# Kernel tuning notes

Hardware: AMD Instinct MI355X
Metric: run time of the kernel (lower is better)

## Reference

```python
import jax, jax.numpy as jnp
import numpy as np

N, E = 50000, 800000
D, F, H = 128, 16, 8
HD = D // H  # head_dim = 16


def setup_inputs() -> dict:
    key = jax.random.key(0)
    ks = jax.random.split(key, 9)
    s = 1.0 / np.sqrt(D)
    return {
        "x": jax.random.normal(ks[0], (N, D), dtype=jnp.float32),
        "edge_index": jax.random.randint(ks[1], (2, E), 0, N, dtype=jnp.int32),
        "edge_attr": jax.random.normal(ks[2], (E, F), dtype=jnp.float32),
        "Wq": jax.random.normal(ks[3], (D, D), dtype=jnp.float32) * s,
        "Wk": jax.random.normal(ks[4], (D, D), dtype=jnp.float32) * s,
        "Wv": jax.random.normal(ks[5], (D, D), dtype=jnp.float32) * s,
        "We": jax.random.normal(ks[6], (H, F), dtype=jnp.float32) * (1.0 / np.sqrt(F)),
        "Wo": jax.random.normal(ks[7], (D, D), dtype=jnp.float32) * s,
        "bo": jax.random.normal(ks[8], (D,), dtype=jnp.float32) * 0.01,
    }


def reference(x, edge_index, edge_attr, Wq, Wk, Wv, We, Wo, bo):
    src, tgt = edge_index[0], edge_index[1]
    # Projections, reshaped to (N, H, HD)
    Q = (x @ Wq.T).reshape(N, H, HD)
    K = (x @ Wk.T).reshape(N, H, HD)
    V = (x @ Wv.T).reshape(N, H, HD)
    # Per-edge scores: (E, H)
    attn = jnp.einsum('ehd,ehd->eh', Q[src], K[tgt]) / jnp.sqrt(jnp.float32(HD))
    attn = attn + edge_attr @ We.T  # edge bias (E, H)
    # Scatter softmax over target node segments
    m = jax.ops.segment_max(attn, tgt, num_segments=N)  # (N, H)
    m = jnp.where(jnp.isneginf(m), 0.0, m)
    e = jnp.exp(attn - m[tgt])
    ssum = jax.ops.segment_sum(e, tgt, num_segments=N)  # (N, H)
    ssum = jnp.where(ssum == 0.0, 1.0, ssum)
    a = e / ssum[tgt]  # (E, H); dropout p=0.0 -> identity
    # Weighted scatter-add aggregation: (N, D)
    out_edge = (a[:, :, None] * V[tgt]).reshape(E, D)
    out = jnp.zeros((N, D), dtype=x.dtype).at[tgt].add(out_edge)
    return out @ Wo.T + bo
```

## Files before the change

### kernel.cpp

```cpp
#include <hip/hip_runtime.h>
#include <hip/hip_bf16.h>

#define NN 50000
#define NE 800000
#define DD 128
#define MARK_BLOCKS 782


typedef __bf16 bf16x8 __attribute__((ext_vector_type(8)));
typedef float floatx4 __attribute__((ext_vector_type(4)));

__global__ __launch_bounds__(256) void prep_kernel(
        const int* __restrict__ tgt,
        const float* __restrict__ Wo,
        const float* __restrict__ Wv,
        unsigned char* __restrict__ mask,
        __hip_bfloat16* __restrict__ Wc) {
    const int b = blockIdx.x;
    if (b < MARK_BLOCKS) {
        int i4 = b * 256 + threadIdx.x;
        if (i4 < NE / 4) {
            int4 t = reinterpret_cast<const int4*>(tgt)[i4];
            mask[t.x] = 1; mask[t.y] = 1; mask[t.z] = 1; mask[t.w] = 1;
        }
    } else {
        int idx = (b - MARK_BLOCKS) * 256 + threadIdx.x;
        int j = idx >> 7, k = idx & 127;
        float acc = 0.f;
#pragma unroll 8
        for (int t = 0; t < DD; ++t)
            acc += Wo[j * DD + t] * Wv[t * DD + k];
        Wc[idx] = __float2bfloat16(acc);
    }
}

#define LDSW (DD + 8)

__global__ __launch_bounds__(512) void final_gemm_kernel(
        const float* __restrict__ x,
        const __hip_bfloat16* __restrict__ Wc,
        const unsigned char* __restrict__ mask,
        const float* __restrict__ bo,
        float* __restrict__ out) {
    __shared__ __hip_bfloat16 sWc[DD * LDSW];

    const int tid = threadIdx.x;

    for (int it = 0; it < 4; ++it) {
        int chunk = it * 512 + tid;
        int row = chunk >> 4;
        int c = chunk & 15;
        uint4 v = *reinterpret_cast<const uint4*>(Wc + row * DD + c * 8);
        *reinterpret_cast<uint4*>(&sWc[row * LDSW + c * 8]) = v;
    }
    __syncthreads();

    const int wave = tid >> 6;
    const int lane = tid & 63;
    const int l15 = lane & 15;
    const int quad = lane >> 4;
    const long rowBase = (long)blockIdx.x * 128 + wave * 16;

    floatx4 acc[8];
#pragma unroll
    for (int nf = 0; nf < 8; ++nf) acc[nf] = (floatx4){0.f, 0.f, 0.f, 0.f};

    long arow = rowBase + l15;
    if (arow > NN - 1) arow = NN - 1;
    const float* xrow = x + arow * DD;
#pragma unroll
    for (int ks = 0; ks < 4; ++ks) {
        const int kOff = ks * 32 + quad * 8;
        floatx4 lo = *reinterpret_cast<const floatx4*>(xrow + kOff);
        floatx4 hi = *reinterpret_cast<const floatx4*>(xrow + kOff + 4);
        bf16x8 afrag;
#pragma unroll
        for (int j = 0; j < 4; ++j) { afrag[j] = (__bf16)lo[j]; afrag[4 + j] = (__bf16)hi[j]; }
#pragma unroll
        for (int nf = 0; nf < 8; ++nf) {
            const bf16x8 bfrag = *reinterpret_cast<const bf16x8*>(
                &sWc[(nf * 16 + l15) * LDSW + kOff]);
            acc[nf] = __builtin_amdgcn_mfma_f32_16x16x32_bf16(afrag, bfrag, acc[nf], 0, 0, 0);
        }
    }

    float bov[8];
#pragma unroll
    for (int nf = 0; nf < 8; ++nf) bov[nf] = bo[nf * 16 + l15];

#pragma unroll
    for (int r = 0; r < 4; ++r) {
        long grow = rowBase + quad * 4 + r;
        if (grow < NN) {
            float mv = (mask[grow] == 1) ? 1.0f : 0.0f;
#pragma unroll
            for (int nf = 0; nf < 8; ++nf) {
                out[grow * DD + nf * 16 + l15] = acc[nf][r] * mv + bov[nf];
            }
        }
    }
}

extern "C" void kernel_launch(void* const* d_in, const int* in_sizes, int n_in,
                              void* d_out, int out_size, void* d_ws, size_t ws_size,
                              hipStream_t stream) {
    const float* x        = (const float*)d_in[0];
    const int* edge_index = (const int*)d_in[1];
    const float* Wv       = (const float*)d_in[5];
    const float* Wo       = (const float*)d_in[7];
    const float* bo       = (const float*)d_in[8];
    float* out = (float*)d_out;

    unsigned char* mask = (unsigned char*)d_ws;
    __hip_bfloat16* Wc  = (__hip_bfloat16*)((char*)d_ws + 50176);

    prep_kernel<<<MARK_BLOCKS + 64, 256, 0, stream>>>(edge_index + NE, Wo, Wv, mask, Wc);
    final_gemm_kernel<<<(NN + 127) / 128, 512, 0, stream>>>(x, Wc, mask, bo, out);
}
```

Before: 129.6 us.

## Fuse mask/weight prep and GEMM into one cooperative kernel with grid sync

Merges the target-mask marking and Wo·Wv weight-combine prep into the GEMM kernel, launched cooperatively with a grid-wide barrier between phases. This removes a separate kernel launch and the inter-kernel gap. It falls back to the original two-kernel path if cooperative launch fails. The grid sync and the occupancy limits of cooperative launch add their own overhead.

New measurement: 303.3 us. 134% more time.

```diff
diff --git a/kernel.cpp b/kernel.cpp
--- a/kernel.cpp
+++ b/kernel.cpp
@@ -1,65 +1,33 @@
 #include <hip/hip_runtime.h>
 #include <hip/hip_bf16.h>
+#include <hip/hip_cooperative_groups.h>
+
+namespace cg = cooperative_groups;
 
 #define NN 50000
 #define NE 800000
 #define DD 128
+#define GEMM_BLOCKS 391
 #define MARK_BLOCKS 782
 
 
 typedef __bf16 bf16x8 __attribute__((ext_vector_type(8)));
 typedef float floatx4 __attribute__((ext_vector_type(4)));
 
-__global__ __launch_bounds__(256) void prep_kernel(
-        const int* __restrict__ tgt,
-        const float* __restrict__ Wo,
-        const float* __restrict__ Wv,
-        unsigned char* __restrict__ mask,
-        __hip_bfloat16* __restrict__ Wc) {
-    const int b = blockIdx.x;
-    if (b < MARK_BLOCKS) {
-        int i4 = b * 256 + threadIdx.x;
-        if (i4 < NE / 4) {
-            int4 t = reinterpret_cast<const int4*>(tgt)[i4];
-            mask[t.x] = 1; mask[t.y] = 1; mask[t.z] = 1; mask[t.w] = 1;
-        }
-    } else {
-        int idx = (b - MARK_BLOCKS) * 256 + threadIdx.x;
-        int j = idx >> 7, k = idx & 127;
-        float acc = 0.f;
-#pragma unroll 8
-        for (int t = 0; t < DD; ++t)
-            acc += Wo[j * DD + t] * Wv[t * DD + k];
-        Wc[idx] = __float2bfloat16(acc);
-    }
-}
-
 #define LDSW (DD + 8)
 
-__global__ __launch_bounds__(512) void final_gemm_kernel(
+__device__ __forceinline__ void gemm_tile(
+        int tile, int tid,
         const float* __restrict__ x,
-        const __hip_bfloat16* __restrict__ Wc,
+        const __hip_bfloat16* __restrict__ sWc,
         const unsigned char* __restrict__ mask,
         const float* __restrict__ bo,
         float* __restrict__ out) {
-    __shared__ __hip_bfloat16 sWc[DD * LDSW];
-
-    const int tid = threadIdx.x;
-
-    for (int it = 0; it < 4; ++it) {
-        int chunk = it * 512 + tid;
-        int row = chunk >> 4;
-        int c = chunk & 15;
-        uint4 v = *reinterpret_cast<const uint4*>(Wc + row * DD + c * 8);
-        *reinterpret_cast<uint4*>(&sWc[row * LDSW + c * 8]) = v;
-    }
-    __syncthreads();
-
     const int wave = tid >> 6;
     const int lane = tid & 63;
     const int l15 = lane & 15;
     const int quad = lane >> 4;
-    const long rowBase = (long)blockIdx.x * 128 + wave * 16;
+    const long rowBase = (long)tile * 128 + wave * 16;
 
     floatx4 acc[8];
 #pragma unroll
@@ -101,6 +69,94 @@
     }
 }
 
+__global__ __launch_bounds__(512, 4) void fused_kernel(
+        const int* __restrict__ tgt,
+        const float* __restrict__ Wo,
+        const float* __restrict__ Wv,
+        const float* __restrict__ x,
+        unsigned char* __restrict__ mask,
+        __hip_bfloat16* __restrict__ Wc,
+        const float* __restrict__ bo,
+        float* __restrict__ out) {
+    __shared__ __hip_bfloat16 sWc[DD * LDSW];
+    const int tid = threadIdx.x;
+    const int blk = blockIdx.x;
+
+    {
+        int i4 = blk * 512 + tid;
+        if (i4 < NE / 4) {
+            int4 t = reinterpret_cast<const int4*>(tgt)[i4];
+            mask[t.x] = 1; mask[t.y] = 1; mask[t.z] = 1; mask[t.w] = 1;
+        }
+    }
+    if (blk < 64 && tid < 256) {
+        int idx = blk * 256 + tid;
+        int j = idx >> 7, k = idx & 127;
+        float acc = 0.f;
+#pragma unroll 16
+        for (int t = 0; t < DD; ++t)
+            acc += Wo[j * DD + t] * Wv[t * DD + k];
+        Wc[idx] = __float2bfloat16(acc);
+    }
+
+    __threadfence();
+    cg::this_grid().sync();
+
+    for (int it = 0; it < 4; ++it) {
+        int chunk = it * 512 + tid;
+        int row = chunk >> 4;
+        int c = chunk & 15;
+        uint4 v = *reinterpret_cast<const uint4*>(Wc + row * DD + c * 8);
+        *reinterpret_cast<uint4*>(&sWc[row * LDSW + c * 8]) = v;
+    }
+    __syncthreads();
+
+    gemm_tile(blk, tid, x, sWc, mask, bo, out);
+}
+
+__global__ __launch_bounds__(256) void prep_kernel(
+        const int* __restrict__ tgt,
+        const float* __restrict__ Wo,
+        const float* __restrict__ Wv,
+        unsigned char* __restrict__ mask,
+        __hip_bfloat16* __restrict__ Wc) {
+    const int b = blockIdx.x;
+    if (b < MARK_BLOCKS) {
+        int i4 = b * 256 + threadIdx.x;
+        if (i4 < NE / 4) {
+            int4 t = reinterpret_cast<const int4*>(tgt)[i4];
+            mask[t.x] = 1; mask[t.y] = 1; mask[t.z] = 1; mask[t.w] = 1;
+        }
+    } else {
+        int idx = (b - MARK_BLOCKS) * 256 + threadIdx.x;
+        int j = idx >> 7, k = idx & 127;
+        float acc = 0.f;
+#pragma unroll 8
+        for (int t = 0; t < DD; ++t)
+            acc += Wo[j * DD + t] * Wv[t * DD + k];
+        Wc[idx] = __float2bfloat16(acc);
+    }
+}
+
+__global__ __launch_bounds__(512) void final_gemm_kernel(
+        const float* __restrict__ x,
+        const __hip_bfloat16* __restrict__ Wc,
+        const unsigned char* __restrict__ mask,
+        const float* __restrict__ bo,
+        float* __restrict__ out) {
+    __shared__ __hip_bfloat16 sWc[DD * LDSW];
+    const int tid = threadIdx.x;
+    for (int it = 0; it < 4; ++it) {
+        int chunk = it * 512 + tid;
+        int row = chunk >> 4;
+        int c = chunk & 15;
+        uint4 v = *reinterpret_cast<const uint4*>(Wc + row * DD + c * 8);
+        *reinterpret_cast<uint4*>(&sWc[row * LDSW + c * 8]) = v;
+    }
+    __syncthreads();
+    gemm_tile(blockIdx.x, tid, x, sWc, mask, bo, out);
+}
+
 extern "C" void kernel_launch(void* const* d_in, const int* in_sizes, int n_in,
                               void* d_out, int out_size, void* d_ws, size_t ws_size,
                               hipStream_t stream) {
@@ -114,6 +170,16 @@
     unsigned char* mask = (unsigned char*)d_ws;
     __hip_bfloat16* Wc  = (__hip_bfloat16*)((char*)d_ws + 50176);
 
-    prep_kernel<<<MARK_BLOCKS + 64, 256, 0, stream>>>(edge_index + NE, Wo, Wv, mask, Wc);
-    final_gemm_kernel<<<(NN + 127) / 128, 512, 0, stream>>>(x, Wc, mask, bo, out);
+    const int* tgt = edge_index + NE;
+
+    void* args[] = { (void*)&tgt, (void*)&Wo, (void*)&Wv, (void*)&x,
+                     (void*)&mask, (void*)&Wc, (void*)&bo, (void*)&out };
+    hipError_t err = hipLaunchCooperativeKernel(
+        reinterpret_cast<const void*>(fused_kernel),
+        dim3(GEMM_BLOCKS), dim3(512), args, 0, stream);
+
+    if (err != hipSuccess) {
+        prep_kernel<<<MARK_BLOCKS + 64, 256, 0, stream>>>(tgt, Wo, Wv, mask, Wc);
+        final_gemm_kernel<<<GEMM_BLOCKS, 512, 0, stream>>>(x, Wc, mask, bo, out);
+    }
 }
```
